# Kernel tuning notes

Hardware: AMD Instinct MI355X
Metric: run time of the kernel (lower is better)

## Reference

```python
import jax, jax.numpy as jnp
import numpy as np

IN_F = 512
OUT_F = 256
ALPHA = 0.2  # LeakyReLU negative slope
NEG_INF = -9e15


def setup_inputs() -> dict:
    key = jax.random.key(0)
    k1, k2, k3, k4 = jax.random.split(key, 4)
    N = 8192
    inp = jax.random.normal(k1, (N, IN_F), dtype=jnp.float32)
    adj = jax.random.randint(k2, (N, N), 0, 2, dtype=jnp.int32)
    # xavier_normal with gain=1.414
    std_W = 1.414 * np.sqrt(2.0 / (IN_F + OUT_F))
    W = jax.random.normal(k3, (IN_F, OUT_F), dtype=jnp.float32) * std_W
    std_a = 1.414 * np.sqrt(2.0 / (2 * OUT_F + 1))
    a = jax.random.normal(k4, (2 * OUT_F, 1), dtype=jnp.float32) * std_a
    return {"input": inp, "adj": adj, "W": W, "a": a}


def reference(input, adj, W, a):
    h = input @ W                              # [N, F]
    attn_self = h @ a[:OUT_F]                  # [N, 1]
    attn_neigh = h @ a[OUT_F:]                 # [N, 1]
    dense = attn_self + attn_neigh.T           # [N, N] broadcast add
    dense = jnp.where(dense >= 0, dense, ALPHA * dense)  # leaky relu
    scores = jnp.where(adj > 0, dense, NEG_INF)
    attention = jax.nn.softmax(scores, axis=1)  # dropout p=0.0 -> identity
    h_prime = attention @ h                     # [N, F]
    return jax.nn.elu(h_prime)                  # concat=True branch
```

## Files before the change

kernel.cpp:

```cpp
#include <hip/hip_runtime.h>
#include <hip/hip_bf16.h>
#include <math.h>

#define DEVI static __device__ __forceinline__

using f32x4  = __attribute__((ext_vector_type(4))) float;
using f32x16 = __attribute__((ext_vector_type(16))) float;
using s16x8  = __attribute__((ext_vector_type(8))) short;
using bf16x8 = __attribute__((ext_vector_type(8))) __bf16;
using i32x4  = __attribute__((ext_vector_type(4))) int;
using u32x2  = __attribute__((ext_vector_type(2))) unsigned int;

constexpr int N   = 8192;
constexpr int KIN = 512;
constexpr int F   = 256;

DEVI unsigned f2bf(float f) {
  unsigned u = __builtin_bit_cast(unsigned, f);
  return ((u + 0x7FFFu + ((u >> 16) & 1u)) >> 16) & 0xFFFFu;
}

DEVI unsigned cvtpk(float lo, float hi) {
  unsigned r;
  asm("v_cvt_pk_bf16_f32 %0, %1, %2" : "=v"(r) : "v"(lo), "v"(hi));
  return r;
}

DEVI f32x16 mfma32(s16x8 a, s16x8 b, f32x16 c) {
  return __builtin_amdgcn_mfma_f32_32x32x16_bf16(
      __builtin_bit_cast(bf16x8, a), __builtin_bit_cast(bf16x8, b), c, 0, 0, 0);
}

DEVI void gload16(const void* g, void* lds_uniform) {
  __builtin_amdgcn_global_load_lds(
      (const __attribute__((address_space(1))) unsigned*)g,
      (__attribute__((address_space(3))) unsigned*)lds_uniform, 16, 0, 0);
}

__global__ __launch_bounds__(256) void k_cast(const float* __restrict__ src,
                                              unsigned short* __restrict__ dst,
                                              int n8) {
  int t = blockIdx.x * 256 + threadIdx.x;
  if (t >= n8) return;
  const f32x4* p = (const f32x4*)(src + (size_t)t * 8);
  f32x4 v0 = p[0], v1 = p[1];
  s16x8 o;
  o[0] = (short)f2bf(v0[0]); o[1] = (short)f2bf(v0[1]);
  o[2] = (short)f2bf(v0[2]); o[3] = (short)f2bf(v0[3]);
  o[4] = (short)f2bf(v1[0]); o[5] = (short)f2bf(v1[1]);
  o[6] = (short)f2bf(v1[2]); o[7] = (short)f2bf(v1[3]);
  *(s16x8*)(dst + (size_t)t * 8) = o;
}

__global__ __launch_bounds__(256) void k_prep_w(const float* __restrict__ W,
                                                unsigned short* __restrict__ Wt) {
  int t = blockIdx.x * 256 + threadIdx.x;
  int c = t >> 6, k0 = (t & 63) * 8;
  s16x8 o;
#pragma unroll
  for (int i = 0; i < 8; ++i) o[i] = (short)f2bf(W[(size_t)(k0 + i) * F + c]);
  *(s16x8*)(Wt + (size_t)c * KIN + k0) = o;
}

__global__ __launch_bounds__(512) void k_gemm1(const unsigned short* __restrict__ inpb,
                                               const unsigned short* __restrict__ Wt,
                                               const float* __restrict__ a_vec,
                                               unsigned short* __restrict__ Ht,
                                               float* __restrict__ E, float* __restrict__ E5,
                                               float* __restrict__ Fv, float* __restrict__ F5v) {
  __shared__ __align__(16) char lds[4096 + 32768 + 2048];
  char* ldsA = lds;
  char* ldsW = lds + 4096;
  float* red = (float*)(lds + 36864);
  int tid = threadIdx.x, w = tid >> 6, l = tid & 63;
  int r0 = blockIdx.x * 32;
  f32x16 acc;
#pragma unroll
  for (int i = 0; i < 16; ++i) acc[i] = 0.f;

  int lrow8 = l >> 3;
  int koffB = ((l & 7) ^ lrow8) * 8;
  int ra = l & 31, kb = (l >> 5) * 8;
  int colw = w * 32 + ra;

  for (int it = 0; it < 8; ++it) {
    int k0 = it * 64;
    __syncthreads();
    if (w < 4) {
      int row = 8 * w + lrow8;
      gload16(inpb + (size_t)(r0 + row) * KIN + k0 + koffB, ldsA + w * 1024);
    }
#pragma unroll
    for (int qi = 0; qi < 4; ++qi) {
      int q = 4 * w + qi;
      int c = 8 * q + lrow8;
      gload16(Wt + (size_t)c * KIN + k0 + koffB, ldsW + q * 1024);
    }
    __syncthreads();
    s16x8 av[4], bv[4];
#pragma unroll
    for (int kf = 0; kf < 4; ++kf) {
      int kk2 = (kf * 16 + kb) * 2;
      av[kf] = *(const s16x8*)(ldsA + ra * 128 + (kk2 ^ ((ra & 7) << 4)));
      bv[kf] = *(const s16x8*)(ldsW + colw * 128 + (kk2 ^ ((colw & 7) << 4)));
    }
#pragma unroll
    for (int kf = 0; kf < 4; ++kf) acc = mfma32(av[kf], bv[kf], acc);
  }

  float a1 = a_vec[colw], a2 = a_vec[256 + colw];
  int rquad = (l >> 5) * 4;
#pragma unroll
  for (int g = 0; g < 4; ++g) {
    int rowb = g * 8 + rquad;
    unsigned h0 = f2bf(acc[g * 4 + 0]), h1 = f2bf(acc[g * 4 + 1]);
    unsigned h2 = f2bf(acc[g * 4 + 2]), h3 = f2bf(acc[g * 4 + 3]);
    u32x2 pk;
    pk[0] = h0 | (h1 << 16);
    pk[1] = h2 | (h3 << 16);
    *(u32x2*)(Ht + (size_t)colw * N + r0 + rowb) = pk;
  }
#pragma unroll
  for (int g = 0; g < 16; ++g) {
    float vs = acc[g] * a1;
    float vn = acc[g] * a2;
#pragma unroll
    for (int m = 1; m <= 16; m <<= 1) {
      vs += __shfl_xor(vs, m, 64);
      vn += __shfl_xor(vn, m, 64);
    }
    if ((l & 31) == 0) {
      int row = (g & 3) + 8 * (g >> 2) + rquad;
      red[row * 8 + w] = vs;
      red[256 + row * 8 + w] = vn;
    }
  }
  __syncthreads();
  if (tid < 32) {
    float s = 0.f, n2 = 0.f;
#pragma unroll
    for (int i = 0; i < 8; ++i) { s += red[tid * 8 + i]; n2 += red[256 + tid * 8 + i]; }
    E[r0 + tid]   = expf(s);
    E5[r0 + tid]  = expf(0.2f * s);
    Fv[r0 + tid]  = expf(n2);
    F5v[r0 + tid] = expf(0.2f * n2);
  }
}

__global__ __launch_bounds__(512, 4) void k_phase2(const int* __restrict__ adj,
                                                   const unsigned short* __restrict__ Ht,
                                                   const float* __restrict__ E,
                                                   const float* __restrict__ E5,
                                                   const float* __restrict__ Fv,
                                                   const float* __restrict__ F5v,
                                                   float* __restrict__ pacc,
                                                   float* __restrict__ ps) {
  __shared__ __align__(16) char lds[65536 + 8192];
  char* ldsH = lds;
  char* ldsP = lds + 65536;

  const int tid = threadIdx.x, w = tid >> 6, l = tid & 63;
  const int rb = blockIdx.x >> 1, ks = blockIdx.x & 1;
  const int r0 = rb * 32;
  const int jb = ks * 4096;

  const int r = tid >> 4, cch = tid & 15;
  const float Er = E[r0 + r], E5r = E5[r0 + r];
  float s_part = 0.f;
  const int*   __restrict__ adjR = adj + (size_t)(r0 + r) * N + jb + cch * 4;
  const float* __restrict__ FvR  = Fv  + jb + cch * 4;
  const float* __restrict__ GvR  = F5v + jb + cch * 4;
  const int pw_byte = r * 128 + ((cch * 8) ^ ((r & 7) << 4));

  const int lrow8 = l >> 3;
  const int koffB = ((l & 7) ^ lrow8) * 8;
  const int ra = l & 31;
  const int kb = (l >> 5) * 8;
  const int colw = w * 32 + (l & 31);

  f32x16 acc;
#pragma unroll
  for (int i = 0; i < 16; ++i) acc[i] = 0.f;

  i32x4 ad = *(const i32x4*)(adjR);
  f32x4 fc = *(const f32x4*)(FvR);
  f32x4 gc = *(const f32x4*)(GvR);
#pragma unroll
  for (int qi = 0; qi < 4; ++qi) {
    int q = 4 * w + qi;
    int c = 8 * q + lrow8;
    gload16(Ht + (size_t)c * N + jb + koffB, ldsH + q * 1024);
  }

  for (int it = 0; it < 64; ++it) {
    const int cur = it & 1;
    char* Hc = ldsH + cur * 32768;
    char* Hn = ldsH + (cur ^ 1) * 32768;
    char* Pc = ldsP + cur * 4096;
    const int itn = (it + 1) & 63;
    const int jn = itn * 64;

    i32x4 adn = *(const i32x4*)(adjR + jn);
    f32x4 fn = *(const f32x4*)(FvR + jn);
    f32x4 gn = *(const f32x4*)(GvR + jn);

    {
      float p0 = (ad[0] != 0) ? fmaxf(Er * fc[0], E5r * gc[0]) : 0.f;
      float p1 = (ad[1] != 0) ? fmaxf(Er * fc[1], E5r * gc[1]) : 0.f;
      float p2 = (ad[2] != 0) ? fmaxf(Er * fc[2], E5r * gc[2]) : 0.f;
      float p3 = (ad[3] != 0) ? fmaxf(Er * fc[3], E5r * gc[3]) : 0.f;
      s_part += (p0 + p1) + (p2 + p3);
      u32x2 pk;
      pk[0] = cvtpk(p0, p1);
      pk[1] = cvtpk(p2, p3);
      *(u32x2*)(Pc + pw_byte) = pk;
    }

    asm volatile("s_waitcnt vmcnt(3) lgkmcnt(0)" ::: "memory");
    __builtin_amdgcn_s_barrier();

    s16x8 av[4], bv[4];
#pragma unroll
    for (int kf = 0; kf < 4; ++kf) {
      int kk2 = (kf * 16 + kb) * 2;
      av[kf] = *(const s16x8*)(Pc + ra * 128 + (kk2 ^ ((ra & 7) << 4)));
      bv[kf] = *(const s16x8*)(Hc + colw * 128 + (kk2 ^ ((colw & 7) << 4)));
    }
    asm volatile("s_waitcnt lgkmcnt(0)" ::: "memory");
    __builtin_amdgcn_sched_barrier(0);

#pragma unroll
    for (int qi = 0; qi < 4; ++qi) {
      int q = 4 * w + qi;
      int c = 8 * q + lrow8;
      gload16(Ht + (size_t)c * N + jb + jn + koffB, Hn + q * 1024);
    }

    acc = mfma32(av[0], bv[0], acc);
    acc = mfma32(av[1], bv[1], acc);
    acc = mfma32(av[2], bv[2], acc);
    acc = mfma32(av[3], bv[3], acc);

    ad = adn; fc = fn; gc = gn;
  }

  float s = s_part;
#pragma unroll
  for (int m = 1; m <= 8; m <<= 1) s += __shfl_xor(s, m, 64);
  if (cch == 0) ps[(size_t)ks * N + r0 + r] = s;

  float* po = pacc + (size_t)ks * N * F;
#pragma unroll
  for (int g = 0; g < 16; ++g) {
    int orow = (g & 3) + 8 * (g >> 2) + 4 * (l >> 5);
    po[(size_t)(r0 + orow) * F + colw] = acc[g];
  }
}

__global__ __launch_bounds__(256) void k_combine(const float* __restrict__ pacc,
                                                 const float* __restrict__ ps,
                                                 float* __restrict__ out) {
  int t = blockIdx.x * 256 + threadIdx.x;
  size_t idx = (size_t)t * 4;
  int row = (int)(idx >> 8);
  f32x4 a0 = *(const f32x4*)(pacc + idx);
  f32x4 a1 = *(const f32x4*)(pacc + (size_t)N * F + idx);
  float inv = 1.f / (ps[row] + ps[N + row]);
  f32x4 o;
#pragma unroll
  for (int i = 0; i < 4; ++i) {
    float v = (a0[i] + a1[i]) * inv;
    o[i] = v > 0.f ? v : expm1f(v);
  }
  *(f32x4*)(out + idx) = o;
}

extern "C" void kernel_launch(void* const* d_in, const int* in_sizes, int n_in,
                              void* d_out, int out_size, void* d_ws, size_t ws_size,
                              hipStream_t stream) {
  const float* input = (const float*)d_in[0];
  const int*   adj   = (const int*)d_in[1];
  const float* W     = (const float*)d_in[2];
  const float* a     = (const float*)d_in[3];
  float* out = (float*)d_out;
  char* ws = (char*)d_ws;

  unsigned short* inpb = (unsigned short*)(ws);
  unsigned short* Wt   = (unsigned short*)(ws + 8388608);
  unsigned short* Ht   = (unsigned short*)(ws + 8650752);
  float* E    = (float*)(ws + 12845056);
  float* E5   = (float*)(ws + 12877824);
  float* Fv   = (float*)(ws + 12910592);
  float* F5   = (float*)(ws + 12943360);
  float* ps   = (float*)(ws + 12976128);
  float* pacc = (float*)(ws + 13041664);

  hipLaunchKernelGGL(k_cast,   dim3(2048), dim3(256), 0, stream, input, inpb, 524288);
  hipLaunchKernelGGL(k_prep_w, dim3(64),   dim3(256), 0, stream, W, Wt);
  hipLaunchKernelGGL(k_gemm1,  dim3(256),  dim3(512), 0, stream, inpb, Wt, a, Ht, E, E5, Fv, F5);
  hipLaunchKernelGGL(k_phase2, dim3(512),  dim3(512), 0, stream, adj, Ht, E, E5, Fv, F5, pacc, ps);
  hipLaunchKernelGGL(k_combine,dim3(2048), dim3(256), 0, stream, pacc, ps, out);
}
```

Before: 134.6 us.

## Enlarge attention tile to 64 rows, split keys four ways, store partials in bf16

The aggregation kernel now computes 64 output rows per block with two MFMA accumulators per wave, and splits the neighbour dimension four ways instead of two. This halves how often each H tile is loaded relative to the adjacency work. The per-neighbour exponent pair is packed into one bf16x2 word, and the split partial sums are stored as bf16 to cut workspace traffic. The combine kernel then sums four partials. A single P buffer with an extra barrier replaces the double-buffered one. Keeping the exponent factors and partials in bf16 lowers numerical precision.

Result: faster. 117.3 us (-12.8%).

```diff
diff --git a/kernel.cpp b/kernel.cpp
--- a/kernel.cpp
+++ b/kernel.cpp
@@ -10,6 +10,7 @@
 using bf16x8 = __attribute__((ext_vector_type(8))) __bf16;
 using i32x4  = __attribute__((ext_vector_type(4))) int;
 using u32x2  = __attribute__((ext_vector_type(2))) unsigned int;
+using u32x4  = __attribute__((ext_vector_type(4))) unsigned int;
 
 constexpr int N   = 8192;
 constexpr int KIN = 512;
@@ -19,6 +20,9 @@
   unsigned u = __builtin_bit_cast(unsigned, f);
   return ((u + 0x7FFFu + ((u >> 16) & 1u)) >> 16) & 0xFFFFu;
 }
+
+DEVI float bfLO(unsigned u) { return __builtin_bit_cast(float, (u & 0xFFFFu) << 16); }
+DEVI float bfHI(unsigned u) { return __builtin_bit_cast(float, u & 0xFFFF0000u); }
 
 DEVI unsigned cvtpk(float lo, float hi) {
   unsigned r;
@@ -67,7 +71,7 @@
                                                const float* __restrict__ a_vec,
                                                unsigned short* __restrict__ Ht,
                                                float* __restrict__ E, float* __restrict__ E5,
-                                               float* __restrict__ Fv, float* __restrict__ F5v) {
+                                               unsigned* __restrict__ FG) {
   __shared__ __align__(16) char lds[4096 + 32768 + 2048];
   char* ldsA = lds;
   char* ldsW = lds + 4096;
@@ -140,10 +144,9 @@
     float s = 0.f, n2 = 0.f;
 #pragma unroll
     for (int i = 0; i < 8; ++i) { s += red[tid * 8 + i]; n2 += red[256 + tid * 8 + i]; }
-    E[r0 + tid]   = expf(s);
-    E5[r0 + tid]  = expf(0.2f * s);
-    Fv[r0 + tid]  = expf(n2);
-    F5v[r0 + tid] = expf(0.2f * n2);
+    E[r0 + tid]  = expf(s);
+    E5[r0 + tid] = expf(0.2f * s);
+    FG[r0 + tid] = f2bf(expf(n2)) | (f2bf(expf(0.2f * n2)) << 16);
   }
 }
 
@@ -151,40 +154,42 @@
                                                    const unsigned short* __restrict__ Ht,
                                                    const float* __restrict__ E,
                                                    const float* __restrict__ E5,
-                                                   const float* __restrict__ Fv,
-                                                   const float* __restrict__ F5v,
-                                                   float* __restrict__ pacc,
+                                                   const unsigned* __restrict__ FG,
+                                                   unsigned short* __restrict__ pacc,
                                                    float* __restrict__ ps) {
   __shared__ __align__(16) char lds[65536 + 8192];
   char* ldsH = lds;
   char* ldsP = lds + 65536;
 
   const int tid = threadIdx.x, w = tid >> 6, l = tid & 63;
-  const int rb = blockIdx.x >> 1, ks = blockIdx.x & 1;
-  const int r0 = rb * 32;
-  const int jb = ks * 4096;
-
-  const int r = tid >> 4, cch = tid & 15;
+  const int rb = blockIdx.x >> 2, ks = blockIdx.x & 3;
+  const int r0 = rb * 64;
+  const int jb = ks * 2048;
+
+  const int r = tid >> 3, jc8 = (tid & 7) * 8;
   const float Er = E[r0 + r], E5r = E5[r0 + r];
   float s_part = 0.f;
-  const int*   __restrict__ adjR = adj + (size_t)(r0 + r) * N + jb + cch * 4;
-  const float* __restrict__ FvR  = Fv  + jb + cch * 4;
-  const float* __restrict__ GvR  = F5v + jb + cch * 4;
-  const int pw_byte = r * 128 + ((cch * 8) ^ ((r & 7) << 4));
+  const int*      __restrict__ adjR = adj + (size_t)(r0 + r) * N + jb + jc8;
+  const unsigned* __restrict__ fgR  = FG + jb + jc8;
+  const int pw_byte = r * 128 + ((jc8 * 2) ^ ((r & 7) << 4));
 
   const int lrow8 = l >> 3;
   const int koffB = ((l & 7) ^ lrow8) * 8;
-  const int ra = l & 31;
-  const int kb = (l >> 5) * 8;
-  const int colw = w * 32 + (l & 31);
-
-  f32x16 acc;
-#pragma unroll
-  for (int i = 0; i < 16; ++i) acc[i] = 0.f;
-
-  i32x4 ad = *(const i32x4*)(adjR);
-  f32x4 fc = *(const f32x4*)(FvR);
-  f32x4 gc = *(const f32x4*)(GvR);
+  const int rg = w >> 2, fg = w & 3;
+  const int ra = rg * 32 + (l & 31);
+  const int khb = (l >> 5) * 16;
+  const int col0 = fg * 64 + (l & 31);
+  const int col1 = col0 + 32;
+  const int swz = (l & 7) << 4;
+
+  f32x16 acc0, acc1;
+#pragma unroll
+  for (int i = 0; i < 16; ++i) { acc0[i] = 0.f; acc1[i] = 0.f; }
+
+  i32x4 ad0 = *(const i32x4*)(adjR);
+  i32x4 ad1 = *(const i32x4*)(adjR + 4);
+  u32x4 fgc0 = *(const u32x4*)(fgR);
+  u32x4 fgc1 = *(const u32x4*)(fgR + 4);
 #pragma unroll
   for (int qi = 0; qi < 4; ++qi) {
     int q = 4 * w + qi;
@@ -192,42 +197,35 @@
     gload16(Ht + (size_t)c * N + jb + koffB, ldsH + q * 1024);
   }
 
-  for (int it = 0; it < 64; ++it) {
-    const int cur = it & 1;
-    char* Hc = ldsH + cur * 32768;
-    char* Hn = ldsH + (cur ^ 1) * 32768;
-    char* Pc = ldsP + cur * 4096;
-    const int itn = (it + 1) & 63;
+  for (int it = 0; it < 32; ++it) {
+    char* Hc = ldsH + (it & 1) * 32768;
+    char* Hn = ldsH + ((it & 1) ^ 1) * 32768;
+    const int itn = (it + 1) & 31;
     const int jn = itn * 64;
 
-    i32x4 adn = *(const i32x4*)(adjR + jn);
-    f32x4 fn = *(const f32x4*)(FvR + jn);
-    f32x4 gn = *(const f32x4*)(GvR + jn);
+    i32x4 nad0 = *(const i32x4*)(adjR + jn);
+    i32x4 nad1 = *(const i32x4*)(adjR + jn + 4);
+    u32x4 nfg0 = *(const u32x4*)(fgR + jn);
+    u32x4 nfg1 = *(const u32x4*)(fgR + jn + 4);
 
     {
-      float p0 = (ad[0] != 0) ? fmaxf(Er * fc[0], E5r * gc[0]) : 0.f;
-      float p1 = (ad[1] != 0) ? fmaxf(Er * fc[1], E5r * gc[1]) : 0.f;
-      float p2 = (ad[2] != 0) ? fmaxf(Er * fc[2], E5r * gc[2]) : 0.f;
-      float p3 = (ad[3] != 0) ? fmaxf(Er * fc[3], E5r * gc[3]) : 0.f;
-      s_part += (p0 + p1) + (p2 + p3);
-      u32x2 pk;
-      pk[0] = cvtpk(p0, p1);
-      pk[1] = cvtpk(p2, p3);
-      *(u32x2*)(Pc + pw_byte) = pk;
-    }
-
-    asm volatile("s_waitcnt vmcnt(3) lgkmcnt(0)" ::: "memory");
+      float p0 = (ad0[0] != 0) ? fmaxf(Er * bfLO(fgc0[0]), E5r * bfHI(fgc0[0])) : 0.f;
+      float p1 = (ad0[1] != 0) ? fmaxf(Er * bfLO(fgc0[1]), E5r * bfHI(fgc0[1])) : 0.f;
+      float p2 = (ad0[2] != 0) ? fmaxf(Er * bfLO(fgc0[2]), E5r * bfHI(fgc0[2])) : 0.f;
+      float p3 = (ad0[3] != 0) ? fmaxf(Er * bfLO(fgc0[3]), E5r * bfHI(fgc0[3])) : 0.f;
+      float p4 = (ad1[0] != 0) ? fmaxf(Er * bfLO(fgc1[0]), E5r * bfHI(fgc1[0])) : 0.f;
+      float p5 = (ad1[1] != 0) ? fmaxf(Er * bfLO(fgc1[1]), E5r * bfHI(fgc1[1])) : 0.f;
+      float p6 = (ad1[2] != 0) ? fmaxf(Er * bfLO(fgc1[2]), E5r * bfHI(fgc1[2])) : 0.f;
+      float p7 = (ad1[3] != 0) ? fmaxf(Er * bfLO(fgc1[3]), E5r * bfHI(fgc1[3])) : 0.f;
+      s_part += ((p0 + p1) + (p2 + p3)) + ((p4 + p5) + (p6 + p7));
+      u32x4 pk;
+      pk[0] = cvtpk(p0, p1); pk[1] = cvtpk(p2, p3);
+      pk[2] = cvtpk(p4, p5); pk[3] = cvtpk(p6, p7);
+      *(u32x4*)(ldsP + pw_byte) = pk;
+    }
+
+    asm volatile("s_waitcnt vmcnt(4) lgkmcnt(0)" ::: "memory");
     __builtin_amdgcn_s_barrier();
-
-    s16x8 av[4], bv[4];
-#pragma unroll
-    for (int kf = 0; kf < 4; ++kf) {
-      int kk2 = (kf * 16 + kb) * 2;
-      av[kf] = *(const s16x8*)(Pc + ra * 128 + (kk2 ^ ((ra & 7) << 4)));
-      bv[kf] = *(const s16x8*)(Hc + colw * 128 + (kk2 ^ ((colw & 7) << 4)));
-    }
-    asm volatile("s_waitcnt lgkmcnt(0)" ::: "memory");
-    __builtin_amdgcn_sched_barrier(0);
 
 #pragma unroll
     for (int qi = 0; qi < 4; ++qi) {
@@ -236,40 +234,56 @@
       gload16(Ht + (size_t)c * N + jb + jn + koffB, Hn + q * 1024);
     }
 
-    acc = mfma32(av[0], bv[0], acc);
-    acc = mfma32(av[1], bv[1], acc);
-    acc = mfma32(av[2], bv[2], acc);
-    acc = mfma32(av[3], bv[3], acc);
-
-    ad = adn; fc = fn; gc = gn;
+#pragma unroll
+    for (int kt = 0; kt < 4; ++kt) {
+      int kk2 = kt * 32 + khb;
+      s16x8 av = *(const s16x8*)(ldsP + ra * 128 + (kk2 ^ swz));
+      s16x8 b0 = *(const s16x8*)(Hc + col0 * 128 + (kk2 ^ swz));
+      s16x8 b1 = *(const s16x8*)(Hc + col1 * 128 + (kk2 ^ swz));
+      acc0 = mfma32(av, b0, acc0);
+      acc1 = mfma32(av, b1, acc1);
+    }
+
+    asm volatile("s_waitcnt lgkmcnt(0)" ::: "memory");
+    __builtin_amdgcn_s_barrier();
+
+    ad0 = nad0; ad1 = nad1; fgc0 = nfg0; fgc1 = nfg1;
   }
 
   float s = s_part;
 #pragma unroll
-  for (int m = 1; m <= 8; m <<= 1) s += __shfl_xor(s, m, 64);
-  if (cch == 0) ps[(size_t)ks * N + r0 + r] = s;
-
-  float* po = pacc + (size_t)ks * N * F;
+  for (int m = 1; m <= 4; m <<= 1) s += __shfl_xor(s, m, 64);
+  if ((tid & 7) == 0) ps[(size_t)ks * N + r0 + r] = s;
+
+  unsigned short* po = pacc + (size_t)ks * N * F;
 #pragma unroll
   for (int g = 0; g < 16; ++g) {
-    int orow = (g & 3) + 8 * (g >> 2) + 4 * (l >> 5);
-    po[(size_t)(r0 + orow) * F + colw] = acc[g];
-  }
-}
-
-__global__ __launch_bounds__(256) void k_combine(const float* __restrict__ pacc,
+    int orow = rg * 32 + (g & 3) + 8 * (g >> 2) + 4 * (l >> 5);
+    po[(size_t)(r0 + orow) * F + col0] = (unsigned short)f2bf(acc0[g]);
+    po[(size_t)(r0 + orow) * F + col1] = (unsigned short)f2bf(acc1[g]);
+  }
+}
+
+__global__ __launch_bounds__(256) void k_combine(const unsigned short* __restrict__ pacc,
                                                  const float* __restrict__ ps,
                                                  float* __restrict__ out) {
   int t = blockIdx.x * 256 + threadIdx.x;
   size_t idx = (size_t)t * 4;
   int row = (int)(idx >> 8);
-  f32x4 a0 = *(const f32x4*)(pacc + idx);
-  f32x4 a1 = *(const f32x4*)(pacc + (size_t)N * F + idx);
-  float inv = 1.f / (ps[row] + ps[N + row]);
+  f32x4 sum;
+#pragma unroll
+  for (int i = 0; i < 4; ++i) sum[i] = 0.f;
+#pragma unroll
+  for (int k = 0; k < 4; ++k) {
+    u32x2 q = *(const u32x2*)(pacc + (size_t)k * N * F + idx);
+    sum[0] += bfLO(q[0]) * 1.f; sum[1] += bfHI(q[0]);
+    sum[2] += bfLO(q[1]);       sum[3] += bfHI(q[1]);
+  }
+  float inv = 1.f / (ps[row] + ps[N + row] + ps[2 * N + row] + ps[3 * N + row]);
   f32x4 o;
 #pragma unroll
   for (int i = 0; i < 4; ++i) {
-    float v = (a0[i] + a1[i]) * inv;
+    float v = sum[i] * inv;
     o[i] = v > 0.f ? v : expm1f(v);
   }
   *(f32x4*)(out + idx) = o;
@@ -285,19 +299,18 @@
   float* out = (float*)d_out;
   char* ws = (char*)d_ws;
 
+  unsigned short* pacc = (unsigned short*)(ws);
   unsigned short* inpb = (unsigned short*)(ws);
   unsigned short* Wt   = (unsigned short*)(ws + 8388608);
-  unsigned short* Ht   = (unsigned short*)(ws + 8650752);
-  float* E    = (float*)(ws + 12845056);
-  float* E5   = (float*)(ws + 12877824);
-  float* Fv   = (float*)(ws + 12910592);
-  float* F5   = (float*)(ws + 12943360);
-  float* ps   = (float*)(ws + 12976128);
-  float* pacc = (float*)(ws + 13041664);
+  unsigned short* Ht   = (unsigned short*)(ws + 16777216);
+  float*    E  = (float*)(ws + 20971520);
+  float*    E5 = (float*)(ws + 21004288);
+  unsigned* FG = (unsigned*)(ws + 21037056);
+  float*    ps = (float*)(ws + 21069824);
 
   hipLaunchKernelGGL(k_cast,   dim3(2048), dim3(256), 0, stream, input, inpb, 524288);
   hipLaunchKernelGGL(k_prep_w, dim3(64),   dim3(256), 0, stream, W, Wt);
-  hipLaunchKernelGGL(k_gemm1,  dim3(256),  dim3(512), 0, stream, inpb, Wt, a, Ht, E, E5, Fv, F5);
-  hipLaunchKernelGGL(k_phase2, dim3(512),  dim3(512), 0, stream, adj, Ht, E, E5, Fv, F5, pacc, ps);
+  hipLaunchKernelGGL(k_gemm1,  dim3(256),  dim3(512), 0, stream, inpb, Wt, a, Ht, E, E5, FG);
+  hipLaunchKernelGGL(k_phase2, dim3(512),  dim3(512), 0, stream, adj, Ht, E, E5, FG, pacc, ps);
   hipLaunchKernelGGL(k_combine,dim3(2048), dim3(256), 0, stream, pacc, ps, out);
 }
```
